# Kernel optimization log

Hardware: AMD Instinct MI355X
Metric: run time of the kernel (lower is better)

## Reference

```python
import jax, jax.numpy as jnp
import numpy as np


def setup_inputs() -> dict:
    key = jax.random.key(0)
    k1, k2, k3, k4 = jax.random.split(key, 4)
    I, C, H, W = 8, 32, 480, 480
    X = Y = Z = 64
    coordinates = jax.random.normal(k1, (3, X, Y, Z), dtype=jnp.float32)
    images = jax.random.normal(k2, (I, C, H, W), dtype=jnp.float32)
    transformations = jax.random.normal(k3, (I, 3, 4), dtype=jnp.float32)
    T_cw = jax.random.normal(k4, (I, 4, 4), dtype=jnp.float32)
    return {"coordinates": coordinates, "images": images,
            "transformations": transformations, "T_cw": T_cw}


def reference(coordinates, images, transformations, T_cw):
    # coordinates: [3, X, Y, Z] world-space voxel centers
    # images:          [I, C, H, W]
    # transformations: [I, 3, 4] world -> pixel projection
    # T_cw:            [I, 4, 4] world -> camera
    I, C, H, W = images.shape
    _, X, Y, Z = coordinates.shape
    N = X * Y * Z
    coords = coordinates.reshape(3, N).T                      # [N, 3]
    homog = jnp.concatenate([coords, jnp.ones((N, 1), coords.dtype)], axis=-1)  # [N, 4]

    # Project voxels into each image plane
    pix = jnp.einsum('ikl,nl->ink', transformations, homog)   # [I, N, 3]
    z = pix[..., 2]
    eps = jnp.asarray(1e-8, pix.dtype)
    z_safe = jnp.where(jnp.abs(z) < eps, eps, z)
    u = pix[..., 0] / z_safe                                  # [I, N]
    v = pix[..., 1] / z_safe                                  # [I, N]

    # Validity: in front of camera and inside image bounds
    valid = (z > 0) & (u >= 0) & (u <= W - 1) & (v >= 0) & (v <= H - 1)  # [I, N]

    # Nearest-neighbor sampling (grid_sampling_mode='nearest', zeros padding)
    ui = jnp.clip(jnp.round(u), 0, W - 1).astype(jnp.int32)
    vi = jnp.clip(jnp.round(v), 0, H - 1).astype(jnp.int32)
    feats = images[jnp.arange(I)[:, None], :, vi, ui]          # [I, N, C]
    validity = valid.astype(feats.dtype)[..., None]            # [I, N, 1]
    feats = feats * validity

    # Projected depth: z coordinate in each camera frame
    depth = jnp.einsum('il,nl->in', T_cw[:, 2, :], homog)[..., None]  # [I, N, 1]

    # Viewing direction: normalized ray from camera center to voxel
    R = T_cw[:, :3, :3]                                        # [I, 3, 3]
    t = T_cw[:, :3, 3]                                         # [I, 3]
    cam_center = -jnp.einsum('ikl,ik->il', R, t)               # [I, 3] (= -R^T t)
    view_dir = coords[None, :, :] - cam_center[:, None, :]     # [I, N, 3]
    view_dir = view_dir / jnp.linalg.norm(view_dir, axis=-1, keepdims=True).clip(1e-8)

    # Concat channels: features + depth + validity + viewing direction
    out = jnp.concatenate([feats, depth, validity, view_dir], axis=-1)  # [I, N, C+5]
    out = out.transpose(0, 2, 1).reshape(I, C + 5, X, Y, Z)
    return out
```

## Files before the change

### kernel.cpp

```cpp
#include <hip/hip_runtime.h>
#include <math.h>

namespace {

typedef float f32x4 __attribute__((ext_vector_type(4)));

constexpr int NI   = 8;
constexpr int NC   = 32;
constexpr int NH   = 480;
constexpr int NW   = 480;
constexpr int NPTS = 64 * 64 * 64;
constexpr int NOUTC = NC + 5;
constexpr long long HW = (long long)NH * NW;
constexpr int PPT = 4;
constexpr int TPB = 256;

__global__ __launch_bounds__(TPB)
void smear_kernel(const float* __restrict__ coords,
                  const float* __restrict__ images,
                  const float* __restrict__ trans,
                  const float* __restrict__ tcw,
                  float* __restrict__ out)
{
#pragma clang fp contract(off)
    const int img = blockIdx.y;

    __shared__ float s_tr[12];
    __shared__ float s_t2[4];
    __shared__ float s_cam[3];

    const int tid = threadIdx.x;
    if (tid < 12) s_tr[tid] = trans[img * 12 + tid];
    if (tid < 4)  s_t2[tid] = tcw[img * 16 + 8 + tid];
    if (tid < 3) {
        const float* T = tcw + img * 16;
        float cc = T[0 + tid] * T[3] + T[4 + tid] * T[7];
        cc = cc + T[8 + tid] * T[11];
        s_cam[tid] = -cc;
    }
    __syncthreads();

    const int n0 = (blockIdx.x * TPB + tid) * PPT;
    const f32x4 xv = *(const f32x4*)(coords + n0);
    const f32x4 yv = *(const f32x4*)(coords + NPTS + n0);
    const f32x4 zv = *(const f32x4*)(coords + 2 * NPTS + n0);

    int   off[4];
    float validity[4];
    #pragma unroll
    for (int k = 0; k < PPT; ++k) {
        const float x = xv[k], y = yv[k], z = zv[k];
        const float p0 = ((s_tr[0] * x + s_tr[1] * y) + s_tr[2]  * z) + s_tr[3];
        const float p1 = ((s_tr[4] * x + s_tr[5] * y) + s_tr[6]  * z) + s_tr[7];
        const float p2 = ((s_tr[8] * x + s_tr[9] * y) + s_tr[10] * z) + s_tr[11];
        const float zsafe = (fabsf(p2) < 1e-8f) ? 1e-8f : p2;
        const float u = p0 / zsafe;
        const float v = p1 / zsafe;
        const bool valid = (p2 > 0.0f) && (u >= 0.0f) && (u <= (float)(NW - 1))
                                       && (v >= 0.0f) && (v <= (float)(NH - 1));
        const int ui = (int)fminf(fmaxf(rintf(u), 0.0f), (float)(NW - 1));
        const int vi = (int)fminf(fmaxf(rintf(v), 0.0f), (float)(NH - 1));
        off[k]      = valid ? (vi * NW + ui) : 0;
        validity[k] = valid ? 1.0f : 0.0f;
    }

    const float* ib = images + (long long)img * NC * HW;
    float*       ob = out    + (long long)img * NOUTC * NPTS + n0;
    #pragma unroll
    for (int c = 0; c < NC; ++c) {
        const float* ip = ib + (long long)c * HW;
        f32x4 f;
        f[0] = ip[off[0]] * validity[0];
        f[1] = ip[off[1]] * validity[1];
        f[2] = ip[off[2]] * validity[2];
        f[3] = ip[off[3]] * validity[3];
        __builtin_nontemporal_store(f, (f32x4*)(ob + (long long)c * NPTS));
    }

    f32x4 d4, a4, x4, y4, z4;
    #pragma unroll
    for (int k = 0; k < PPT; ++k) {
        const float x = xv[k], y = yv[k], z = zv[k];
        d4[k] = ((s_t2[0] * x + s_t2[1] * y) + s_t2[2] * z) + s_t2[3];
        a4[k] = validity[k];
        const float dx = x - s_cam[0];
        const float dy = y - s_cam[1];
        const float dz = z - s_cam[2];
        float nrm = sqrtf((dx * dx + dy * dy) + dz * dz);
        nrm = fmaxf(nrm, 1e-8f);
        x4[k] = dx / nrm;
        y4[k] = dy / nrm;
        z4[k] = dz / nrm;
    }
    __builtin_nontemporal_store(d4, (f32x4*)(ob + (long long)(NC + 0) * NPTS));
    __builtin_nontemporal_store(a4, (f32x4*)(ob + (long long)(NC + 1) * NPTS));
    __builtin_nontemporal_store(x4, (f32x4*)(ob + (long long)(NC + 2) * NPTS));
    __builtin_nontemporal_store(y4, (f32x4*)(ob + (long long)(NC + 3) * NPTS));
    __builtin_nontemporal_store(z4, (f32x4*)(ob + (long long)(NC + 4) * NPTS));
}

}

extern "C" void kernel_launch(void* const* d_in, const int* in_sizes, int n_in,
                              void* d_out, int out_size, void* d_ws, size_t ws_size,
                              hipStream_t stream)
{
    const float* coords = (const float*)d_in[0];
    const float* images = (const float*)d_in[1];
    const float* trans  = (const float*)d_in[2];
    const float* tcw    = (const float*)d_in[3];
    float* out = (float*)d_out;

    dim3 grid(NPTS / (TPB * PPT), NI);
    smear_kernel<<<grid, dim3(TPB), 0, stream>>>(coords, images, trans, tcw, out);
}
```

Measured before the change: 446.8 us.

## Split channel gather across a grid z-dimension of channel groups

```diff
diff --git a/kernel.cpp b/kernel.cpp
--- a/kernel.cpp
+++ b/kernel.cpp
@@ -14,6 +14,8 @@
 constexpr long long HW = (long long)NH * NW;
 constexpr int PPT = 4;
 constexpr int TPB = 256;
+constexpr int CG  = 8;
+constexpr int NGRP = NC / CG + 1;
 
 __global__ __launch_bounds__(TPB)
 void smear_kernel(const float* __restrict__ coords,
@@ -24,6 +26,7 @@
 {
 #pragma clang fp contract(off)
     const int img = blockIdx.y;
+    const int grp = blockIdx.z;
 
     __shared__ float s_tr[12];
     __shared__ float s_t2[4];
@@ -64,39 +67,51 @@
         validity[k] = valid ? 1.0f : 0.0f;
     }
 
-    const float* ib = images + (long long)img * NC * HW;
-    float*       ob = out    + (long long)img * NOUTC * NPTS + n0;
-    #pragma unroll
-    for (int c = 0; c < NC; ++c) {
-        const float* ip = ib + (long long)c * HW;
-        f32x4 f;
-        f[0] = ip[off[0]] * validity[0];
-        f[1] = ip[off[1]] * validity[1];
-        f[2] = ip[off[2]] * validity[2];
-        f[3] = ip[off[3]] * validity[3];
-        __builtin_nontemporal_store(f, (f32x4*)(ob + (long long)c * NPTS));
+    float* ob = out + (long long)img * NOUTC * NPTS + n0;
+
+    if (grp < NGRP - 1) {
+        const int c0 = grp * CG;
+        const float* ib = images + ((long long)img * NC + c0) * HW;
+        float fv[CG][4];
+        #pragma unroll
+        for (int c = 0; c < CG; ++c) {
+            const float* ip = ib + (long long)c * HW;
+            fv[c][0] = ip[off[0]];
+            fv[c][1] = ip[off[1]];
+            fv[c][2] = ip[off[2]];
+            fv[c][3] = ip[off[3]];
+        }
+        #pragma unroll
+        for (int c = 0; c < CG; ++c) {
+            f32x4 f;
+            f[0] = fv[c][0] * validity[0];
+            f[1] = fv[c][1] * validity[1];
+            f[2] = fv[c][2] * validity[2];
+            f[3] = fv[c][3] * validity[3];
+            __builtin_nontemporal_store(f, (f32x4*)(ob + (long long)(c0 + c) * NPTS));
+        }
+    } else {
+        f32x4 d4, a4, x4, y4, z4;
+        #pragma unroll
+        for (int k = 0; k < PPT; ++k) {
+            const float x = xv[k], y = yv[k], z = zv[k];
+            d4[k] = ((s_t2[0] * x + s_t2[1] * y) + s_t2[2] * z) + s_t2[3];
+            a4[k] = validity[k];
+            const float dx = x - s_cam[0];
+            const float dy = y - s_cam[1];
+            const float dz = z - s_cam[2];
+            float nrm = sqrtf((dx * dx + dy * dy) + dz * dz);
+            nrm = fmaxf(nrm, 1e-8f);
+            x4[k] = dx / nrm;
+            y4[k] = dy / nrm;
+            z4[k] = dz / nrm;
+        }
+        __builtin_nontemporal_store(d4, (f32x4*)(ob + (long long)(NC + 0) * NPTS));
+        __builtin_nontemporal_store(a4, (f32x4*)(ob + (long long)(NC + 1) * NPTS));
+        __builtin_nontemporal_store(x4, (f32x4*)(ob + (long long)(NC + 2) * NPTS));
+        __builtin_nontemporal_store(y4, (f32x4*)(ob + (long long)(NC + 3) * NPTS));
+        __builtin_nontemporal_store(z4, (f32x4*)(ob + (long long)(NC + 4) * NPTS));
     }
-
-    f32x4 d4, a4, x4, y4, z4;
-    #pragma unroll
-    for (int k = 0; k < PPT; ++k) {
-        const float x = xv[k], y = yv[k], z = zv[k];
-        d4[k] = ((s_t2[0] * x + s_t2[1] * y) + s_t2[2] * z) + s_t2[3];
-        a4[k] = validity[k];
-        const float dx = x - s_cam[0];
-        const float dy = y - s_cam[1];
-        const float dz = z - s_cam[2];
-        float nrm = sqrtf((dx * dx + dy * dy) + dz * dz);
-        nrm = fmaxf(nrm, 1e-8f);
-        x4[k] = dx / nrm;
-        y4[k] = dy / nrm;
-        z4[k] = dz / nrm;
-    }
-    __builtin_nontemporal_store(d4, (f32x4*)(ob + (long long)(NC + 0) * NPTS));
-    __builtin_nontemporal_store(a4, (f32x4*)(ob + (long long)(NC + 1) * NPTS));
-    __builtin_nontemporal_store(x4, (f32x4*)(ob + (long long)(NC + 2) * NPTS));
-    __builtin_nontemporal_store(y4, (f32x4*)(ob + (long long)(NC + 3) * NPTS));
-    __builtin_nontemporal_store(z4, (f32x4*)(ob + (long long)(NC + 4) * NPTS));
 }
 
 }
@@ -111,6 +126,6 @@
     const float* tcw    = (const float*)d_in[3];
     float* out = (float*)d_out;
 
-    dim3 grid(NPTS / (TPB * PPT), NI);
+    dim3 grid(NPTS / (TPB * PPT), NI, NGRP);
     smear_kernel<<<grid, dim3(TPB), 0, stream>>>(coords, images, trans, tcw, out);
 }
```

After: 451.0 us. Within noise of the previous version (+0.9%).
